# Kernel optimization log

Measured on AMD Instinct MI355X. Metric: run time of the kernel, lower is better.

The kernel has to match this reference:

```python
import jax, jax.numpy as jnp
import numpy as np

B, C, H, W = 4, 256, 64, 64
IC = C // 2  # inter_channels default = in_channels // 2


def setup_inputs() -> dict:
    key = jax.random.key(0)
    ks = jax.random.split(key, 7)
    x = jax.random.normal(ks[0], (B, C, H, W), dtype=jnp.float32)
    s = 0.02
    Wq = jax.random.normal(ks[1], (IC, C), dtype=jnp.float32) * s
    bq = jnp.zeros((IC,), dtype=jnp.float32)
    Wk = jax.random.normal(ks[2], (IC, C), dtype=jnp.float32) * s
    bk = jnp.zeros((IC,), dtype=jnp.float32)
    Wv = jax.random.normal(ks[3], (C, C), dtype=jnp.float32) * s
    bv = jnp.zeros((C,), dtype=jnp.float32)
    gamma = jnp.full((1,), 0.1, dtype=jnp.float32)  # nn.Parameter; init 0 in torch, 0.1 here for nontrivial grads
    return {"x": x, "Wq": Wq, "bq": bq, "Wk": Wk, "bk": bk, "Wv": Wv, "bv": bv, "gamma": gamma}


def reference(x, Wq, bq, Wk, bk, Wv, bv, gamma):
    b, c, h, w = x.shape
    n = h * w
    # 1x1 conv projections == per-pixel linear layers
    q = jnp.einsum('bchw,oc->bohw', x, Wq) + bq[None, :, None, None]  # [B,IC,H,W]
    k = jnp.einsum('bchw,oc->bohw', x, Wk) + bk[None, :, None, None]
    v = jnp.einsum('bchw,oc->bohw', x, Wv) + bv[None, :, None, None]  # [B,C,H,W]
    q = q.reshape(b, IC, n).transpose(0, 2, 1)  # [B,N,IC]
    k = k.reshape(b, IC, n)                     # [B,IC,N]
    v = v.reshape(b, c, n)                      # [B,C,N]
    scale = jnp.asarray(IC, x.dtype) ** -0.5
    energy = jnp.einsum('bni,bim->bnm', q, k) * scale  # [B,N,N]
    attn = jax.nn.softmax(energy, axis=-1)             # dropout is identity in eval
    # torch: out = bmm(value, attention.transpose(-1,-2)) -> out[b,c,i] = sum_j v[b,c,j]*attn[b,i,j]
    out = jnp.einsum('bcj,bij->bci', v, attn).reshape(b, c, h, w)
    return gamma[0] * out + 2.0 * x
```

## Files before the change

kernel.cpp:

```cpp
#include <hip/hip_runtime.h>
#include <stdint.h>


#define Bn 4
#define Cn 256
#define ICn 128
#define Nn 4096

typedef __attribute__((ext_vector_type(8))) short bf16x8;
typedef __attribute__((ext_vector_type(4))) float f32x4;
typedef __attribute__((ext_vector_type(16))) float f32x16;

__device__ __forceinline__ unsigned short f2bf(float f) {
  union { float f; uint32_t u; } v; v.f = f;
  uint32_t r = (v.u + 0x7fffu + ((v.u >> 16) & 1u)) >> 16;
  return (unsigned short)r;
}

__device__ __forceinline__ uint32_t pk4_fp8(float a, float b, float c, float d) {
  int r = 0;
  r = __builtin_amdgcn_cvt_pk_fp8_f32(a, b, r, false);
  r = __builtin_amdgcn_cvt_pk_fp8_f32(c, d, r, true);
  return (uint32_t)r;
}

__global__ __launch_bounds__(256) void cvt_weights(const float* __restrict__ Wq,
                                                   const float* __restrict__ Wk,
                                                   const float* __restrict__ Wv,
                                                   unsigned short* __restrict__ wbf) {
  int t = blockIdx.x * 256 + threadIdx.x;
  int tile = t >> 9;
  int kk = (t >> 6) & 7;
  int lane = t & 63;
  const float* W; int row;
  if (tile < 8)       { W = Wq; row = tile * 16 + (lane & 15); }
  else if (tile < 16) { W = Wk; row = (tile - 8) * 16 + (lane & 15); }
  else                { W = Wv; row = (tile - 16) * 16 + (lane & 15); }
  const float* src = W + (size_t)row * Cn + kk * 32 + (lane >> 4) * 8;
  float4 f0 = *(const float4*)src;
  float4 f1 = *(const float4*)(src + 4);
  ushort4 o0, o1;
  o0.x = f2bf(f0.x); o0.y = f2bf(f0.y); o0.z = f2bf(f0.z); o0.w = f2bf(f0.w);
  o1.x = f2bf(f1.x); o1.y = f2bf(f1.y); o1.z = f2bf(f1.z); o1.w = f2bf(f1.w);
  *(ushort4*)(wbf + (size_t)t * 8)     = o0;
  *(ushort4*)(wbf + (size_t)t * 8 + 4) = o1;
}

__global__ __launch_bounds__(256, 2) void proj_kernel(const float* __restrict__ x,
                                                      const unsigned short* __restrict__ wbf,
                                                      const float* __restrict__ bq,
                                                      const float* __restrict__ bk,
                                                      const float* __restrict__ bv,
                                                      uint8_t* __restrict__ qF,
                                                      uint8_t* __restrict__ kF,
                                                      uint8_t* __restrict__ vF) {
  const int b = blockIdx.y;
  const int ntile = blockIdx.x;
  const int px0 = ntile * 32;
  const int tid = threadIdx.x;
  const int lane = tid & 63;
  const int w = tid >> 6;
  const int c0 = lane & 15, g = lane >> 4;

  __shared__ __align__(16) unsigned short xT[32][264];

  #pragma unroll
  for (int t = 0; t < 8; ++t) {
    int c = (tid >> 3) + t * 32;
    int i8 = tid & 7;
    float4 f4 = *(const float4*)(x + ((size_t)(b * Cn + c)) * Nn + px0 + i8 * 4);
    xT[i8 * 4 + 0][c] = f2bf(f4.x);
    xT[i8 * 4 + 1][c] = f2bf(f4.y);
    xT[i8 * 4 + 2][c] = f2bf(f4.z);
    xT[i8 * 4 + 3][c] = f2bf(f4.w);
  }
  __syncthreads();

  bf16x8 a[2][8];
  #pragma unroll
  for (int h = 0; h < 2; ++h)
    #pragma unroll
    for (int kk = 0; kk < 8; ++kk)
      a[h][kk] = *(const bf16x8*)&xT[h * 16 + c0][kk * 32 + g * 8];

  f32x4 zero = {0.f, 0.f, 0.f, 0.f};

  if (w < 2) {
    const float* bias = (w == 0) ? bq : bk;
    uint8_t* dst = (w == 0) ? qF : kF;
    #pragma unroll
    for (int otl = 0; otl < 8; ++otl) {
      bf16x8 wf[8];
      #pragma unroll
      for (int kk = 0; kk < 8; ++kk)
        wf[kk] = *(const bf16x8*)(wbf + (((size_t)(w * 8 + otl) * 8 + kk) << 9) + lane * 8);
      float4 bz = *(const float4*)(bias + otl * 16 + g * 4);
      #pragma unroll
      for (int h = 0; h < 2; ++h) {
        f32x4 acc = zero;
        #pragma unroll
        for (int kk = 0; kk < 8; ++kk)
          acc = __builtin_amdgcn_mfma_f32_16x16x32_bf16(wf[kk], a[h][kk], acc, 0, 0, 0);
        uint32_t d = pk4_fp8(acc[0] + bz.x, acc[1] + bz.y, acc[2] + bz.z, acc[3] + bz.w);
        size_t idx = (((((size_t)b * 128 + ntile) * 4 + (otl >> 1)) * 2 + (g >> 1)) * 32
                      + (h * 16 + c0)) * 16 + (otl & 1) * 8 + (g & 1) * 4;
        *(uint32_t*)(dst + idx) = d;
      }
    }
  } else {
    const int vt0 = (w - 2) * 8;
    #pragma unroll
    for (int vt = 0; vt < 8; ++vt) {
      const int vtg = vt0 + vt;
      bf16x8 wf[8];
      #pragma unroll
      for (int kk = 0; kk < 8; ++kk)
        wf[kk] = *(const bf16x8*)(wbf + (((size_t)(16 + vtg) * 8 + kk) << 9) + lane * 8);
      const float bias = bv[vtg * 16 + c0];
      #pragma unroll
      for (int h = 0; h < 2; ++h) {
        f32x4 acc = zero;
        #pragma unroll
        for (int kk = 0; kk < 8; ++kk)
          acc = __builtin_amdgcn_mfma_f32_16x16x32_bf16(a[h][kk], wf[kk], acc, 0, 0, 0);
        uint32_t d = pk4_fp8(acc[0] + bias, acc[1] + bias, acc[2] + bias, acc[3] + bias);
        size_t idx = ((((size_t)b * 128 + ntile) * 8 + (vtg >> 1)) * 64
                      + (g >> 1) * 32 + (vtg & 1) * 16 + c0) * 16 + h * 8 + (g & 1) * 4;
        *(uint32_t*)(vF + idx) = d;
      }
    }
  }
}

__global__ __launch_bounds__(256, 2) void attn_kernel(const uint8_t* __restrict__ qF,
                                                      const uint8_t* __restrict__ kF,
                                                      const uint8_t* __restrict__ vF,
                                                      const float* __restrict__ x,
                                                      const float* __restrict__ gamma,
                                                      float* __restrict__ out) {
  const int blk = blockIdx.x;
  const int b = (blk & 7) >> 1;
  const int rg = (blk >> 3) | ((blk & 1) << 6);
  const int n0 = rg * 32;
  const int tid = threadIdx.x;
  const int L = tid & 63;
  const int ks = tid >> 6;
  const int l31 = L & 31, l5 = L >> 5;
  const bool lo = (l5 == 0);
  const float scale = 0.08838834764831845f;

  __shared__ float obuf[256][33];
  __shared__ float lsum[4][32];

  long qf[8];
  {
    const uint8_t* qp = qF + ((size_t)(b * 128 + rg) << 12) + (l5 * 32 + l31) * 16;
    #pragma unroll
    for (int t = 0; t < 4; ++t) {
      union { uint4 u4; struct { uint64_t lo, hi; } s; } u;
      u.u4 = *(const uint4*)(qp + t * 1024);
      qf[2 * t] = (long)u.s.lo; qf[2 * t + 1] = (long)u.s.hi;
    }
  }

  f32x16 oacc[8];
  #pragma unroll
  for (int ct = 0; ct < 8; ++ct)
    #pragma unroll
    for (int i = 0; i < 16; ++i) oacc[ct][i] = 0.f;
  float lacc = 0.f;

  const uint8_t* kBase = kF + (((size_t)b * 128) << 12) + (l5 * 32 + l31) * 16;
  const uint8_t* vBase = vF + (((size_t)b * 128) << 13) + (l5 * 32 + l31) * 16;

  for (int it = 0; it < 32; ++it) {
    const int kb = ks * 32 + it;

    f32x16 s;
    #pragma unroll
    for (int i = 0; i < 16; ++i) s[i] = 0.f;
    {
      const uint8_t* kp = kBase + ((size_t)kb << 12);
      #pragma unroll
      for (int t = 0; t < 4; ++t) {
        union { uint4 u4; struct { uint64_t lo, hi; } s; } u;
        u.u4 = *(const uint4*)(kp + t * 1024);
        s = __builtin_amdgcn_mfma_f32_32x32x16_fp8_fp8((long)u.s.lo, qf[2 * t], s, 0, 0, 0);
        s = __builtin_amdgcn_mfma_f32_32x32x16_fp8_fp8((long)u.s.hi, qf[2 * t + 1], s, 0, 0, 0);
      }
    }

    float p[16];
    #pragma unroll
    for (int i = 0; i < 16; ++i) p[i] = __expf(s[i] * scale);
    #pragma unroll
    for (int i = 0; i < 16; ++i) lacc += p[i];
    uint32_t d0 = pk4_fp8(p[0], p[1], p[2], p[3]);
    uint32_t d1 = pk4_fp8(p[4], p[5], p[6], p[7]);
    uint32_t d2 = pk4_fp8(p[8], p[9], p[10], p[11]);
    uint32_t d3 = pk4_fp8(p[12], p[13], p[14], p[15]);

    uint32_t X1 = __shfl_xor(lo ? d1 : d0, 32, 64);
    uint32_t X2 = __shfl_xor(lo ? d3 : d2, 32, 64);
    long f0 = lo ? (long)(((uint64_t)X1 << 32) | d0) : (long)(((uint64_t)d1 << 32) | X1);
    long f1 = lo ? (long)(((uint64_t)X2 << 32) | d2) : (long)(((uint64_t)d3 << 32) | X2);

    const uint8_t* vp = vBase + ((size_t)kb << 13);
    #pragma unroll
    for (int ct = 0; ct < 8; ++ct) {
      union { uint4 u4; struct { uint64_t lo, hi; } s; } u;
      u.u4 = *(const uint4*)(vp + ct * 1024);
      oacc[ct] = __builtin_amdgcn_mfma_f32_32x32x16_fp8_fp8((long)u.s.lo, f0, oacc[ct], 0, 0, 0);
      oacc[ct] = __builtin_amdgcn_mfma_f32_32x32x16_fp8_fp8((long)u.s.hi, f1, oacc[ct], 0, 0, 0);
    }
  }

  float lfin = lacc + __shfl_xor(lacc, 32, 64);
  if (lo) lsum[ks][l31] = lfin;

  #pragma unroll
  for (int pq = 0; pq < 4; ++pq) {
    __syncthreads();
    if (ks == pq) {
      #pragma unroll
      for (int ct = 0; ct < 8; ++ct) {
        #pragma unroll
        for (int i = 0; i < 16; ++i) {
          int ch = ct * 32 + (i & 3) + 8 * (i >> 2) + 4 * l5;
          if (pq == 0) obuf[ch][l31] = oacc[ct][i];
          else         obuf[ch][l31] += oacc[ct][i];
        }
      }
    }
  }
  __syncthreads();

  const int row = tid & 31;
  const float coef = gamma[0] / (lsum[0][row] + lsum[1][row] + lsum[2][row] + lsum[3][row]);
  #pragma unroll 4
  for (int t = 0; t < 32; ++t) {
    int ch = (tid >> 5) + t * 8;
    size_t off = ((size_t)(b * Cn + ch)) * Nn + n0 + row;
    out[off] = obuf[ch][row] * coef + 2.0f * x[off];
  }
}

extern "C" void kernel_launch(void* const* d_in, const int* in_sizes, int n_in,
                              void* d_out, int out_size, void* d_ws, size_t ws_size,
                              hipStream_t stream) {
  const float* x     = (const float*)d_in[0];
  const float* Wq    = (const float*)d_in[1];
  const float* bq    = (const float*)d_in[2];
  const float* Wk    = (const float*)d_in[3];
  const float* bk    = (const float*)d_in[4];
  const float* Wv    = (const float*)d_in[5];
  const float* bv    = (const float*)d_in[6];
  const float* gamma = (const float*)d_in[7];
  float* out = (float*)d_out;

  uint8_t* qF = (uint8_t*)d_ws;
  uint8_t* kF = qF + (2u << 20);
  uint8_t* vF = kF + (2u << 20);
  unsigned short* wbf = (unsigned short*)(vF + (4u << 20));

  hipLaunchKernelGGL(cvt_weights, dim3(64), dim3(256), 0, stream, Wq, Wk, Wv, wbf);
  hipLaunchKernelGGL(proj_kernel, dim3(128, 4), dim3(256), 0, stream,
                     x, wbf, bq, bk, bv, qF, kF, vF);
  hipLaunchKernelGGL(attn_kernel, dim3(512), dim3(256), 0, stream,
                     qF, kF, vF, x, gamma, out);
}
```

Measured before the change: 144.1 us.

## Double-buffer K tiles via direct global-to-LDS loads and split projection grid

```diff
diff --git a/kernel.cpp b/kernel.cpp
--- a/kernel.cpp
+++ b/kernel.cpp
@@ -22,6 +22,11 @@
   r = __builtin_amdgcn_cvt_pk_fp8_f32(a, b, r, false);
   r = __builtin_amdgcn_cvt_pk_fp8_f32(c, d, r, true);
   return (uint32_t)r;
+}
+
+__device__ __forceinline__ void glds16(const uint8_t* g, uint8_t* l) {
+  __builtin_amdgcn_global_load_lds((const __attribute__((address_space(1))) void*)g,
+                                   (__attribute__((address_space(3))) void*)l, 16, 0, 0);
 }
 
 __global__ __launch_bounds__(256) void cvt_weights(const float* __restrict__ Wq,
@@ -46,7 +51,7 @@
   *(ushort4*)(wbf + (size_t)t * 8 + 4) = o1;
 }
 
-__global__ __launch_bounds__(256, 2) void proj_kernel(const float* __restrict__ x,
+__global__ __launch_bounds__(256, 4) void proj_kernel(const float* __restrict__ x,
                                                       const unsigned short* __restrict__ wbf,
                                                       const float* __restrict__ bq,
                                                       const float* __restrict__ bk,
@@ -57,10 +62,12 @@
   const int b = blockIdx.y;
   const int ntile = blockIdx.x;
   const int px0 = ntile * 32;
+  const int zv = blockIdx.z;
   const int tid = threadIdx.x;
   const int lane = tid & 63;
   const int w = tid >> 6;
   const int c0 = lane & 15, g = lane >> 4;
+  const float hscale = 0.2973017787506803f;
 
   __shared__ __align__(16) unsigned short xT[32][264];
 
@@ -85,15 +92,19 @@
 
   f32x4 zero = {0.f, 0.f, 0.f, 0.f};
 
-  if (w < 2) {
-    const float* bias = (w == 0) ? bq : bk;
-    uint8_t* dst = (w == 0) ? qF : kF;
-    #pragma unroll
-    for (int otl = 0; otl < 8; ++otl) {
+  if (zv == 0) {
+    const int isq = (w < 2);
+    const float* bias = isq ? bq : bk;
+    uint8_t* dst = isq ? qF : kF;
+    const int t0 = (w & 1) * 4;
+    #pragma unroll
+    for (int oi = 0; oi < 4; ++oi) {
+      const int otl = t0 + oi;
+      const int wt = (isq ? 0 : 8) + otl;
       bf16x8 wf[8];
       #pragma unroll
       for (int kk = 0; kk < 8; ++kk)
-        wf[kk] = *(const bf16x8*)(wbf + (((size_t)(w * 8 + otl) * 8 + kk) << 9) + lane * 8);
+        wf[kk] = *(const bf16x8*)(wbf + (((size_t)wt * 8 + kk) << 9) + lane * 8);
       float4 bz = *(const float4*)(bias + otl * 16 + g * 4);
       #pragma unroll
       for (int h = 0; h < 2; ++h) {
@@ -101,17 +112,17 @@
         #pragma unroll
         for (int kk = 0; kk < 8; ++kk)
           acc = __builtin_amdgcn_mfma_f32_16x16x32_bf16(wf[kk], a[h][kk], acc, 0, 0, 0);
-        uint32_t d = pk4_fp8(acc[0] + bz.x, acc[1] + bz.y, acc[2] + bz.z, acc[3] + bz.w);
+        uint32_t d = pk4_fp8((acc[0] + bz.x) * hscale, (acc[1] + bz.y) * hscale,
+                             (acc[2] + bz.z) * hscale, (acc[3] + bz.w) * hscale);
         size_t idx = (((((size_t)b * 128 + ntile) * 4 + (otl >> 1)) * 2 + (g >> 1)) * 32
                       + (h * 16 + c0)) * 16 + (otl & 1) * 8 + (g & 1) * 4;
         *(uint32_t*)(dst + idx) = d;
       }
     }
   } else {
-    const int vt0 = (w - 2) * 8;
-    #pragma unroll
-    for (int vt = 0; vt < 8; ++vt) {
-      const int vtg = vt0 + vt;
+    #pragma unroll
+    for (int oi = 0; oi < 4; ++oi) {
+      const int vtg = w * 4 + oi;
       bf16x8 wf[8];
       #pragma unroll
       for (int kk = 0; kk < 8; ++kk)
@@ -147,14 +158,16 @@
   const int ks = tid >> 6;
   const int l31 = L & 31, l5 = L >> 5;
   const bool lo = (l5 == 0);
-  const float scale = 0.08838834764831845f;
-
-  __shared__ float obuf[256][33];
+
+  __shared__ __align__(16) union SM {
+    uint8_t kst[4][2][4096];
+    float obuf[256][33];
+  } sm;
   __shared__ float lsum[4][32];
 
   long qf[8];
   {
-    const uint8_t* qp = qF + ((size_t)(b * 128 + rg) << 12) + (l5 * 32 + l31) * 16;
+    const uint8_t* qp = qF + ((size_t)(b * 128 + rg) << 12) + L * 16;
     #pragma unroll
     for (int t = 0; t < 4; ++t) {
       union { uint4 u4; struct { uint64_t lo, hi; } s; } u;
@@ -170,29 +183,58 @@
     for (int i = 0; i < 16; ++i) oacc[ct][i] = 0.f;
   float lacc = 0.f;
 
-  const uint8_t* kBase = kF + (((size_t)b * 128) << 12) + (l5 * 32 + l31) * 16;
-  const uint8_t* vBase = vF + (((size_t)b * 128) << 13) + (l5 * 32 + l31) * 16;
+  const uint8_t* kBaseG = kF + (((size_t)b * 128) << 12);
+  const uint8_t* vBase = vF + (((size_t)b * 128) << 13) + L * 16;
+  uint8_t* kst_w = &sm.kst[tid >> 6][0][0];
+
+  {
+    const uint8_t* kp = kBaseG + (((size_t)(ks * 32)) << 12) + L * 16;
+    #pragma unroll
+    for (int c4 = 0; c4 < 4; ++c4)
+      glds16(kp + c4 * 1024, kst_w + c4 * 1024);
+  }
 
   for (int it = 0; it < 32; ++it) {
+    const int cur = it & 1;
     const int kb = ks * 32 + it;
 
+    long kfr[8];
+    {
+      const uint8_t* kl = kst_w + cur * 4096 + L * 16;
+      #pragma unroll
+      for (int c4 = 0; c4 < 4; ++c4) {
+        union { uint4 u4; struct { uint64_t lo, hi; } s; } u;
+        u.u4 = *(const uint4*)(kl + c4 * 1024);
+        kfr[2 * c4] = (long)u.s.lo; kfr[2 * c4 + 1] = (long)u.s.hi;
+      }
+    }
+    __builtin_amdgcn_sched_barrier(0);
+
+    uint4 vv[8];
+    {
+      const uint8_t* vp = vBase + ((size_t)kb << 13);
+      #pragma unroll
+      for (int ct = 0; ct < 8; ++ct) vv[ct] = *(const uint4*)(vp + ct * 1024);
+    }
+    __builtin_amdgcn_sched_barrier(0);
+
+    if (it < 31) {
+      const uint8_t* kp = kBaseG + (((size_t)(kb + 1)) << 12) + L * 16;
+      #pragma unroll
+      for (int c4 = 0; c4 < 4; ++c4)
+        glds16(kp + c4 * 1024, kst_w + (cur ^ 1) * 4096 + c4 * 1024);
+    }
+
     f32x16 s;
     #pragma unroll
     for (int i = 0; i < 16; ++i) s[i] = 0.f;
-    {
-      const uint8_t* kp = kBase + ((size_t)kb << 12);
-      #pragma unroll
-      for (int t = 0; t < 4; ++t) {
-        union { uint4 u4; struct { uint64_t lo, hi; } s; } u;
-        u.u4 = *(const uint4*)(kp + t * 1024);
-        s = __builtin_amdgcn_mfma_f32_32x32x16_fp8_fp8((long)u.s.lo, qf[2 * t], s, 0, 0, 0);
-        s = __builtin_amdgcn_mfma_f32_32x32x16_fp8_fp8((long)u.s.hi, qf[2 * t + 1], s, 0, 0, 0);
-      }
-    }
+    #pragma unroll
+    for (int f = 0; f < 8; ++f)
+      s = __builtin_amdgcn_mfma_f32_32x32x16_fp8_fp8(kfr[f], qf[f], s, 0, 0, 0);
 
     float p[16];
     #pragma unroll
-    for (int i = 0; i < 16; ++i) p[i] = __expf(s[i] * scale);
+    for (int i = 0; i < 16; ++i) p[i] = __expf(s[i]);
     #pragma unroll
     for (int i = 0; i < 16; ++i) lacc += p[i];
     uint32_t d0 = pk4_fp8(p[0], p[1], p[2], p[3]);
@@ -205,11 +247,10 @@
     long f0 = lo ? (long)(((uint64_t)X1 << 32) | d0) : (long)(((uint64_t)d1 << 32) | X1);
     long f1 = lo ? (long)(((uint64_t)X2 << 32) | d2) : (long)(((uint64_t)d3 << 32) | X2);
 
-    const uint8_t* vp = vBase + ((size_t)kb << 13);
     #pragma unroll
     for (int ct = 0; ct < 8; ++ct) {
       union { uint4 u4; struct { uint64_t lo, hi; } s; } u;
-      u.u4 = *(const uint4*)(vp + ct * 1024);
+      u.u4 = vv[ct];
       oacc[ct] = __builtin_amdgcn_mfma_f32_32x32x16_fp8_fp8((long)u.s.lo, f0, oacc[ct], 0, 0, 0);
       oacc[ct] = __builtin_amdgcn_mfma_f32_32x32x16_fp8_fp8((long)u.s.hi, f1, oacc[ct], 0, 0, 0);
     }
@@ -227,8 +268,8 @@
         #pragma unroll
         for (int i = 0; i < 16; ++i) {
           int ch = ct * 32 + (i & 3) + 8 * (i >> 2) + 4 * l5;
-          if (pq == 0) obuf[ch][l31] = oacc[ct][i];
-          else         obuf[ch][l31] += oacc[ct][i];
+          if (pq == 0) sm.obuf[ch][l31] = oacc[ct][i];
+          else         sm.obuf[ch][l31] += oacc[ct][i];
         }
       }
     }
@@ -241,7 +282,7 @@
   for (int t = 0; t < 32; ++t) {
     int ch = (tid >> 5) + t * 8;
     size_t off = ((size_t)(b * Cn + ch)) * Nn + n0 + row;
-    out[off] = obuf[ch][row] * coef + 2.0f * x[off];
+    out[off] = sm.obuf[ch][row] * coef + 2.0f * x[off];
   }
 }
 
@@ -264,7 +305,7 @@
   unsigned short* wbf = (unsigned short*)(vF + (4u << 20));
 
   hipLaunchKernelGGL(cvt_weights, dim3(64), dim3(256), 0, stream, Wq, Wk, Wv, wbf);
-  hipLaunchKernelGGL(proj_kernel, dim3(128, 4), dim3(256), 0, stream,
+  hipLaunchKernelGGL(proj_kernel, dim3(128, 4, 2), dim3(256), 0, stream,
                      x, wbf, bq, bk, bv, qF, kF, vF);
   hipLaunchKernelGGL(attn_kernel, dim3(512), dim3(256), 0, stream,
                      qF, kF, vF, x, gamma, out);
```

Result: slower. 163.6 us (+13.5%).
